# Kernel optimization log

Measured on AMD Instinct MI355X. Metric: run time of the kernel, lower is better.

## Reference

```python
import jax, jax.numpy as jnp
import numpy as np

L2 = (0.01, 0.01)
L1_RATIO = 0.5
EPS = 1e-16


def soft_thresholding(x, t):
    return jnp.sign(x) * jnp.maximum(jnp.abs(x) - t, 0.0)


def update_u(x, u, v, l1, l2, eps=EPS):
    # x: [B,M,N], u: [B,M,R], v: [B,N,R]
    a = jnp.einsum('bmn,bnr->bmr', x, v)      # x @ v            [B,M,R]
    b = jnp.einsum('bnr,bns->brs', v, v)      # v.mT @ v         [B,R,R]
    R = u.shape[-1]

    def step(u_new, r):
        # Gauss-Seidel update of column r using the freshest u_new (sequential dependency)
        br = jnp.take(b, r, axis=-1)                        # b[..., :, r]   [B,R]
        brr = jnp.take(br, r, axis=-1)                      # b[..., r, r]   [B]
        # term2 = u_new[..., indices] @ b[..., indices, r] computed as full matvec minus the r-th term
        term2 = jnp.einsum('bmk,bk->bm', u_new, br) - jnp.take(u_new, r, axis=-1) * brr[:, None]
        num = soft_thresholding(jnp.take(a, r, axis=-1) - term2, l1)   # [B,M]
        den = brr[:, None] + l2                                        # [B,1]
        ur = (num + eps) / (den + eps)
        return u_new.at[..., r].set(ur), None

    u_new, _ = jax.lax.scan(step, u, jnp.arange(R))
    return u_new


def setup_inputs() -> dict:
    key = jax.random.key(0)
    k1, k2, k3 = jax.random.split(key, 3)
    B, M, N, R = 8, 2048, 2048, 32
    x = jax.random.normal(k1, (B, M, N), dtype=jnp.float32)
    u = jax.random.normal(k2, (B, M, R), dtype=jnp.float32)
    v = jax.random.normal(k3, (B, N, R), dtype=jnp.float32)
    return {"x": x, "u": u, "v": v}


def reference(x, u, v):
    M, N = x.shape[-2], x.shape[-1]
    l1_u = L2[0] * L1_RATIO * N
    l2_u = L2[0] * (1.0 - L1_RATIO) * N
    l1_v = L2[1] * L1_RATIO * M
    l2_v = L2[1] * (1.0 - L1_RATIO) * M
    u = update_u(x, u, v, l1_u, l2_u)                              # factor 0
    v = update_u(jnp.swapaxes(x, -1, -2), v, u, l1_v, l2_v)        # factor 1 (update_v)
    return (u, v)
```

## Files before the change

### kernel.cpp

```cpp
#include <hip/hip_runtime.h>
#include <hip/hip_bf16.h>

#define NB 8
#define MD 2048
#define RD 32
#define KSPLIT 4
#define KSL (2048 / KSPLIT)
#define VT_STRIDE 520
#define XT_STRIDE 40

typedef float floatx4 __attribute__((ext_vector_type(4)));
typedef short shortx8 __attribute__((ext_vector_type(8)));

static __device__ __forceinline__ short f2b(float f) {
    __hip_bfloat16 h = __float2bfloat16(f);
    return (short)*reinterpret_cast<unsigned short*>(&h);
}

__global__ __launch_bounds__(256) void bmat_kernel(const float* __restrict__ w,
                                                   float* __restrict__ bmat) {
    int batch = blockIdx.x >> 5;
    int n0 = (blockIdx.x & 31) * 64;
    int t = threadIdx.x;
    __shared__ float ws[64][36];
    const float* wb = w + ((size_t)batch * 2048 + n0) * RD;
#pragma unroll
    for (int i = 0; i < 8; ++i) {
        int idx = t + i * 256;
        ws[idx >> 5][idx & 31] = wb[(idx >> 5) * RD + (idx & 31)];
    }
    __syncthreads();
    int ii = t >> 3;
    int jq = (t & 7) * 4;
    float acc[4] = {0.f, 0.f, 0.f, 0.f};
    for (int n = 0; n < 64; ++n) {
        float wi = ws[n][ii];
        float4 wj = *(const float4*)&ws[n][jq];
        acc[0] = fmaf(wi, wj.x, acc[0]);
        acc[1] = fmaf(wi, wj.y, acc[1]);
        acc[2] = fmaf(wi, wj.z, acc[2]);
        acc[3] = fmaf(wi, wj.w, acc[3]);
    }
    float* bp = bmat + ((size_t)batch * RD + ii) * RD + jq;
#pragma unroll
    for (int c = 0; c < 4; ++c) atomicAdd(bp + c, acc[c]);
}

__global__ __launch_bounds__(256, 4) void gemm1_kernel(const float* __restrict__ x,
                                                       const float* __restrict__ v,
                                                       float* __restrict__ a) {
    __shared__ short wT[32 * VT_STRIDE];
    int bz = blockIdx.x;
    int ks = bz & (KSPLIT - 1);
    int mblk = (bz >> 2) & 31;
    int batch = bz >> 7;
    int t = threadIdx.x;
    int lane = t & 63;
    int wave = t >> 6;

    const float* wb = v + ((size_t)batch * 2048 + ks * KSL) * RD;
#pragma unroll
    for (int i = 0; i < 16; ++i) {
        int idx = t + i * 256;
        int k = idx >> 3;
        int rq = (idx & 7) * 4;
        float4 f = *(const float4*)(wb + (size_t)k * RD + rq);
        wT[(rq + 0) * VT_STRIDE + k] = f2b(f.x);
        wT[(rq + 1) * VT_STRIDE + k] = f2b(f.y);
        wT[(rq + 2) * VT_STRIDE + k] = f2b(f.z);
        wT[(rq + 3) * VT_STRIDE + k] = f2b(f.w);
    }
    __syncthreads();

    int kq = (lane >> 4) * 8;
    const float* xrow =
        x + ((size_t)batch * MD + mblk * 64 + wave * 16 + (lane & 15)) * 2048 + ks * KSL + kq;
    int r0 = (lane & 15) * VT_STRIDE + kq;
    int r1 = ((lane & 15) + 16) * VT_STRIDE + kq;

    floatx4 acc0 = {0.f, 0.f, 0.f, 0.f}, acc1 = {0.f, 0.f, 0.f, 0.f};
    float4 fa = *(const float4*)(xrow);
    float4 fb = *(const float4*)(xrow + 4);
    for (int s = 0; s < KSL / 32; ++s) {
        float4 na = {0, 0, 0, 0}, nb = {0, 0, 0, 0};
        if (s + 1 < KSL / 32) {
            na = *(const float4*)(xrow + (s + 1) * 32);
            nb = *(const float4*)(xrow + (s + 1) * 32 + 4);
        }
        shortx8 af = {f2b(fa.x), f2b(fa.y), f2b(fa.z), f2b(fa.w),
                      f2b(fb.x), f2b(fb.y), f2b(fb.z), f2b(fb.w)};
        shortx8 b0 = *(const shortx8*)&wT[r0 + s * 32];
        shortx8 b1 = *(const shortx8*)&wT[r1 + s * 32];
        acc0 = __builtin_amdgcn_mfma_f32_16x16x32_bf16(af, b0, acc0, 0, 0, 0);
        acc1 = __builtin_amdgcn_mfma_f32_16x16x32_bf16(af, b1, acc1, 0, 0, 0);
        fa = na;
        fb = nb;
    }
    float* ab = a + ((size_t)batch * 2048 + mblk * 64 + wave * 16 + (lane >> 4) * 4) * RD + (lane & 15);
#pragma unroll
    for (int i = 0; i < 4; ++i) {
        atomicAdd(ab + i * RD, acc0[i]);
        atomicAdd(ab + i * RD + 16, acc1[i]);
    }
}

__global__ __launch_bounds__(256, 4) void gemm2_kernel(const float* __restrict__ x,
                                                       const float* __restrict__ u,
                                                       float* __restrict__ a) {
    __shared__ short uT[32 * VT_STRIDE];
    __shared__ short xT[4 * 16 * XT_STRIDE];
    int bz = blockIdx.x;
    int ks = bz & (KSPLIT - 1);
    int nblk = (bz >> 2) & 31;
    int batch = bz >> 7;
    int t = threadIdx.x;
    int lane = t & 63;
    int wave = t >> 6;

    const float* ub = u + ((size_t)batch * 2048 + ks * KSL) * RD;
#pragma unroll
    for (int i = 0; i < 16; ++i) {
        int idx = t + i * 256;
        int k = idx >> 3;
        int rq = (idx & 7) * 4;
        float4 f = *(const float4*)(ub + (size_t)k * RD + rq);
        uT[(rq + 0) * VT_STRIDE + k] = f2b(f.x);
        uT[(rq + 1) * VT_STRIDE + k] = f2b(f.y);
        uT[(rq + 2) * VT_STRIDE + k] = f2b(f.z);
        uT[(rq + 3) * VT_STRIDE + k] = f2b(f.w);
    }
    __syncthreads();

    short* xTw = &xT[wave * 16 * XT_STRIDE];
    int mloc = lane & 31;
    int ng = (lane >> 5) * 8;
    int n0w = nblk * 64 + wave * 16;
    const float* xp = x + ((size_t)batch * 2048 + ks * KSL + mloc) * 2048 + n0w + ng;

    int nl = lane & 15;
    int kq = (lane >> 4) * 8;
    int rA = nl * XT_STRIDE + kq;
    int rB0 = nl * VT_STRIDE + kq;
    int rB1 = (nl + 16) * VT_STRIDE + kq;

    floatx4 acc0 = {0.f, 0.f, 0.f, 0.f}, acc1 = {0.f, 0.f, 0.f, 0.f};
    float4 fa = *(const float4*)xp;
    float4 fb = *(const float4*)(xp + 4);
    for (int s = 0; s < KSL / 32; ++s) {
        xTw[(ng + 0) * XT_STRIDE + mloc] = f2b(fa.x);
        xTw[(ng + 1) * XT_STRIDE + mloc] = f2b(fa.y);
        xTw[(ng + 2) * XT_STRIDE + mloc] = f2b(fa.z);
        xTw[(ng + 3) * XT_STRIDE + mloc] = f2b(fa.w);
        xTw[(ng + 4) * XT_STRIDE + mloc] = f2b(fb.x);
        xTw[(ng + 5) * XT_STRIDE + mloc] = f2b(fb.y);
        xTw[(ng + 6) * XT_STRIDE + mloc] = f2b(fb.z);
        xTw[(ng + 7) * XT_STRIDE + mloc] = f2b(fb.w);
        float4 na = {0, 0, 0, 0}, nb = {0, 0, 0, 0};
        if (s + 1 < KSL / 32) {
            na = *(const float4*)(xp + (size_t)(s + 1) * 32 * 2048);
            nb = *(const float4*)(xp + (size_t)(s + 1) * 32 * 2048 + 4);
        }
        shortx8 af = *(const shortx8*)&xTw[rA];
        shortx8 b0 = *(const shortx8*)&uT[rB0 + s * 32];
        shortx8 b1 = *(const shortx8*)&uT[rB1 + s * 32];
        acc0 = __builtin_amdgcn_mfma_f32_16x16x32_bf16(af, b0, acc0, 0, 0, 0);
        acc1 = __builtin_amdgcn_mfma_f32_16x16x32_bf16(af, b1, acc1, 0, 0, 0);
        fa = na;
        fb = nb;
    }
    float* ab = a + ((size_t)batch * 2048 + n0w + (lane >> 4) * 4) * RD + (lane & 15);
#pragma unroll
    for (int i = 0; i < 4; ++i) {
        atomicAdd(ab + i * RD, acc0[i]);
        atomicAdd(ab + i * RD + 16, acc1[i]);
    }
}

__global__ __launch_bounds__(256) void gs_kernel(const float* __restrict__ uin,
                                                 const float* __restrict__ amat,
                                                 const float* __restrict__ bmat,
                                                 float* __restrict__ uout,
                                                 float l1, float l2) {
    int blk = blockIdx.x;
    int batch = blk >> 3;
    int m = (blk & 7) * 256 + threadIdx.x;
    __shared__ float bs[RD][RD];
    ((float4*)&bs[0][0])[threadIdx.x] =
        ((const float4*)(bmat + (size_t)batch * RD * RD))[threadIdx.x];
    __syncthreads();
    float uv[RD], av[RD];
    const float* up = uin + ((size_t)batch * 2048 + m) * RD;
    const float* ap = amat + ((size_t)batch * 2048 + m) * RD;
#pragma unroll
    for (int q = 0; q < 8; ++q) {
        *(float4*)&uv[q * 4] = *(const float4*)&up[q * 4];
        *(float4*)&av[q * 4] = *(const float4*)&ap[q * 4];
    }
#pragma unroll
    for (int r = 0; r < RD; ++r) {
        float brr = bs[r][r];
        float t2 = -uv[r] * brr;
#pragma unroll
        for (int k = 0; k < RD; ++k) t2 = fmaf(uv[k], bs[r][k], t2);
        float num = av[r] - t2;
        float mag = fmaxf(fabsf(num) - l1, 0.f);
        num = copysignf(mag, num);
        uv[r] = (num + 1e-16f) / (brr + l2 + 1e-16f);
    }
    float* op = uout + ((size_t)batch * 2048 + m) * RD;
#pragma unroll
    for (int q = 0; q < 8; ++q) *(float4*)&op[q * 4] = *(float4*)&uv[q * 4];
}

extern "C" void kernel_launch(void* const* d_in, const int* in_sizes, int n_in,
                              void* d_out, int out_size, void* d_ws, size_t ws_size,
                              hipStream_t stream) {
    const float* x = (const float*)d_in[0];
    const float* u = (const float*)d_in[1];
    const float* v = (const float*)d_in[2];
    float* out_u = (float*)d_out;
    float* out_v = out_u + (size_t)NB * MD * RD;
    float* a_ws = (float*)d_ws;
    float* b_ws = a_ws + (size_t)NB * 2048 * RD;
    const float l1u = 10.24f, l2u = 10.24f;
    const float l1v = 10.24f, l2v = 10.24f;
    size_t abytes = (size_t)NB * 2048 * RD * sizeof(float);
    size_t bbytes = (size_t)NB * RD * RD * sizeof(float);

    hipMemsetAsync(a_ws, 0, abytes + bbytes, stream);
    bmat_kernel<<<NB * 32, 256, 0, stream>>>(v, b_ws);
    gemm1_kernel<<<NB * 32 * KSPLIT, 256, 0, stream>>>(x, v, a_ws);
    gs_kernel<<<NB * 8, 256, 0, stream>>>(u, a_ws, b_ws, out_u, l1u, l2u);

    hipMemsetAsync(a_ws, 0, abytes + bbytes, stream);
    bmat_kernel<<<NB * 32, 256, 0, stream>>>(out_u, b_ws);
    gemm2_kernel<<<NB * 32 * KSPLIT, 256, 0, stream>>>(x, out_u, a_ws);
    gs_kernel<<<NB * 8, 256, 0, stream>>>(v, a_ws, b_ws, out_v, l1v, l2v);
}
```

Baseline: 255.2 us.

## Fuse Gram and GEMM kernels, replace atomics with split-K partial buffers

Merges the Gram-matrix kernel into the GEMM launch by giving the first blocks the bmat work, so the separate bmat kernel and memsets go away. Split-K partials for a and per-slice Gram partials are written with plain stores to separate buffers instead of atomics, and the Gauss-Seidel kernel sums them when it loads them. The GS inner dot product also gets four independent accumulators over float4 LDS reads. This costs more workspace and more reads in the GS kernel, and changes the floating-point summation order.

Measured after the change: 253.7 us (median of 2 runs). Within noise of the previous version (-0.6%).

```diff
diff --git a/kernel.cpp b/kernel.cpp
--- a/kernel.cpp
+++ b/kernel.cpp
@@ -8,6 +8,7 @@
 #define KSL (2048 / KSPLIT)
 #define VT_STRIDE 520
 #define XT_STRIDE 40
+#define ASL ((size_t)NB * 2048 * RD)
 
 typedef float floatx4 __attribute__((ext_vector_type(4)));
 typedef short shortx8 __attribute__((ext_vector_type(8)));
@@ -17,44 +18,50 @@
     return (short)*reinterpret_cast<unsigned short*>(&h);
 }
 
-__global__ __launch_bounds__(256) void bmat_kernel(const float* __restrict__ w,
-                                                   float* __restrict__ bmat) {
-    int batch = blockIdx.x >> 5;
-    int n0 = (blockIdx.x & 31) * 64;
-    int t = threadIdx.x;
-    __shared__ float ws[64][36];
-    const float* wb = w + ((size_t)batch * 2048 + n0) * RD;
+static __device__ __forceinline__ void bmat_part(const float* __restrict__ w,
+                                                 float* __restrict__ bp,
+                                                 int bz, int t, char* smem) {
+    int batch = bz >> 5;
+    int slice = bz & 31;
+    float* ws = (float*)smem;
+    const float* wb = w + ((size_t)batch * 2048 + slice * 64) * RD;
 #pragma unroll
     for (int i = 0; i < 8; ++i) {
         int idx = t + i * 256;
-        ws[idx >> 5][idx & 31] = wb[(idx >> 5) * RD + (idx & 31)];
+        ws[(idx >> 5) * 36 + (idx & 31)] = wb[(idx >> 5) * RD + (idx & 31)];
     }
     __syncthreads();
     int ii = t >> 3;
     int jq = (t & 7) * 4;
-    float acc[4] = {0.f, 0.f, 0.f, 0.f};
+    float a0 = 0.f, a1 = 0.f, a2 = 0.f, a3 = 0.f;
     for (int n = 0; n < 64; ++n) {
-        float wi = ws[n][ii];
-        float4 wj = *(const float4*)&ws[n][jq];
-        acc[0] = fmaf(wi, wj.x, acc[0]);
-        acc[1] = fmaf(wi, wj.y, acc[1]);
-        acc[2] = fmaf(wi, wj.z, acc[2]);
-        acc[3] = fmaf(wi, wj.w, acc[3]);
-    }
-    float* bp = bmat + ((size_t)batch * RD + ii) * RD + jq;
-#pragma unroll
-    for (int c = 0; c < 4; ++c) atomicAdd(bp + c, acc[c]);
-}
-
-__global__ __launch_bounds__(256, 4) void gemm1_kernel(const float* __restrict__ x,
-                                                       const float* __restrict__ v,
-                                                       float* __restrict__ a) {
-    __shared__ short wT[32 * VT_STRIDE];
+        float wi = ws[n * 36 + ii];
+        float4 wj = *(const float4*)&ws[n * 36 + jq];
+        a0 = fmaf(wi, wj.x, a0);
+        a1 = fmaf(wi, wj.y, a1);
+        a2 = fmaf(wi, wj.z, a2);
+        a3 = fmaf(wi, wj.w, a3);
+    }
+    float4 r = {a0, a1, a2, a3};
+    *(float4*)(bp + (((size_t)batch * 32 + slice) * RD + ii) * RD + jq) = r;
+}
+
+__global__ __launch_bounds__(256, 4) void fused1_kernel(const float* __restrict__ x,
+                                                        const float* __restrict__ v,
+                                                        float* __restrict__ ap,
+                                                        float* __restrict__ bp) {
+    __shared__ __align__(16) char smem[32 * VT_STRIDE * 2];
     int bz = blockIdx.x;
+    int t = threadIdx.x;
+    if (bz < NB * 32) {
+        bmat_part(v, bp, bz, t, smem);
+        return;
+    }
+    bz -= NB * 32;
+    short* wT = (short*)smem;
     int ks = bz & (KSPLIT - 1);
     int mblk = (bz >> 2) & 31;
     int batch = bz >> 7;
-    int t = threadIdx.x;
     int lane = t & 63;
     int wave = t >> 6;
 
@@ -96,24 +103,33 @@
         fa = na;
         fb = nb;
     }
-    float* ab = a + ((size_t)batch * 2048 + mblk * 64 + wave * 16 + (lane >> 4) * 4) * RD + (lane & 15);
+    float* ab = ap + ks * ASL +
+                ((size_t)batch * 2048 + mblk * 64 + wave * 16 + (lane >> 4) * 4) * RD +
+                (lane & 15);
 #pragma unroll
     for (int i = 0; i < 4; ++i) {
-        atomicAdd(ab + i * RD, acc0[i]);
-        atomicAdd(ab + i * RD + 16, acc1[i]);
-    }
-}
-
-__global__ __launch_bounds__(256, 4) void gemm2_kernel(const float* __restrict__ x,
-                                                       const float* __restrict__ u,
-                                                       float* __restrict__ a) {
-    __shared__ short uT[32 * VT_STRIDE];
-    __shared__ short xT[4 * 16 * XT_STRIDE];
+        ab[i * RD] = acc0[i];
+        ab[i * RD + 16] = acc1[i];
+    }
+}
+
+__global__ __launch_bounds__(256, 4) void fused2_kernel(const float* __restrict__ x,
+                                                        const float* __restrict__ u,
+                                                        float* __restrict__ ap,
+                                                        float* __restrict__ bp) {
+    __shared__ __align__(16) short smem[32 * VT_STRIDE + 4 * 16 * XT_STRIDE];
     int bz = blockIdx.x;
+    int t = threadIdx.x;
+    if (bz < NB * 32) {
+        bmat_part(u, bp, bz, t, (char*)smem);
+        return;
+    }
+    bz -= NB * 32;
+    short* uT = smem;
+    short* xT = smem + 32 * VT_STRIDE;
     int ks = bz & (KSPLIT - 1);
     int nblk = (bz >> 2) & 31;
     int batch = bz >> 7;
-    int t = threadIdx.x;
     int lane = t & 63;
     int wave = t >> 6;
 
@@ -168,40 +184,68 @@
         fa = na;
         fb = nb;
     }
-    float* ab = a + ((size_t)batch * 2048 + n0w + (lane >> 4) * 4) * RD + (lane & 15);
+    float* ab = ap + ks * ASL +
+                ((size_t)batch * 2048 + n0w + (lane >> 4) * 4) * RD + (lane & 15);
 #pragma unroll
     for (int i = 0; i < 4; ++i) {
-        atomicAdd(ab + i * RD, acc0[i]);
-        atomicAdd(ab + i * RD + 16, acc1[i]);
+        ab[i * RD] = acc0[i];
+        ab[i * RD + 16] = acc1[i];
     }
 }
 
 __global__ __launch_bounds__(256) void gs_kernel(const float* __restrict__ uin,
-                                                 const float* __restrict__ amat,
-                                                 const float* __restrict__ bmat,
+                                                 const float* __restrict__ ap,
+                                                 const float* __restrict__ bp,
                                                  float* __restrict__ uout,
                                                  float l1, float l2) {
     int blk = blockIdx.x;
     int batch = blk >> 3;
     int m = (blk & 7) * 256 + threadIdx.x;
     __shared__ float bs[RD][RD];
-    ((float4*)&bs[0][0])[threadIdx.x] =
-        ((const float4*)(bmat + (size_t)batch * RD * RD))[threadIdx.x];
+    {
+        const float4* bpp = (const float4*)(bp + (size_t)batch * 32 * RD * RD) + threadIdx.x;
+        float4 bacc = {0.f, 0.f, 0.f, 0.f};
+#pragma unroll
+        for (int s = 0; s < 32; ++s) {
+            float4 f = bpp[s * 256];
+            bacc.x += f.x;
+            bacc.y += f.y;
+            bacc.z += f.z;
+            bacc.w += f.w;
+        }
+        ((float4*)&bs[0][0])[threadIdx.x] = bacc;
+    }
     __syncthreads();
     float uv[RD], av[RD];
     const float* up = uin + ((size_t)batch * 2048 + m) * RD;
-    const float* ap = amat + ((size_t)batch * 2048 + m) * RD;
+    const float* app = ap + ((size_t)batch * 2048 + m) * RD;
 #pragma unroll
     for (int q = 0; q < 8; ++q) {
         *(float4*)&uv[q * 4] = *(const float4*)&up[q * 4];
-        *(float4*)&av[q * 4] = *(const float4*)&ap[q * 4];
+        float4 s0 = *(const float4*)(app + q * 4);
+        float4 s1 = *(const float4*)(app + ASL + q * 4);
+        float4 s2 = *(const float4*)(app + 2 * ASL + q * 4);
+        float4 s3 = *(const float4*)(app + 3 * ASL + q * 4);
+        float4 r;
+        r.x = (s0.x + s1.x) + (s2.x + s3.x);
+        r.y = (s0.y + s1.y) + (s2.y + s3.y);
+        r.z = (s0.z + s1.z) + (s2.z + s3.z);
+        r.w = (s0.w + s1.w) + (s2.w + s3.w);
+        *(float4*)&av[q * 4] = r;
     }
 #pragma unroll
     for (int r = 0; r < RD; ++r) {
         float brr = bs[r][r];
-        float t2 = -uv[r] * brr;
-#pragma unroll
-        for (int k = 0; k < RD; ++k) t2 = fmaf(uv[k], bs[r][k], t2);
+        float4 t2v = {0.f, 0.f, 0.f, 0.f};
+#pragma unroll
+        for (int q = 0; q < 8; ++q) {
+            float4 bq = *(const float4*)&bs[r][q * 4];
+            t2v.x = fmaf(uv[q * 4 + 0], bq.x, t2v.x);
+            t2v.y = fmaf(uv[q * 4 + 1], bq.y, t2v.y);
+            t2v.z = fmaf(uv[q * 4 + 2], bq.z, t2v.z);
+            t2v.w = fmaf(uv[q * 4 + 3], bq.w, t2v.w);
+        }
+        float t2 = ((t2v.x + t2v.y) + (t2v.z + t2v.w)) - uv[r] * brr;
         float num = av[r] - t2;
         float mag = fmaxf(fabsf(num) - l1, 0.f);
         num = copysignf(mag, num);
@@ -220,20 +264,15 @@
     const float* v = (const float*)d_in[2];
     float* out_u = (float*)d_out;
     float* out_v = out_u + (size_t)NB * MD * RD;
-    float* a_ws = (float*)d_ws;
-    float* b_ws = a_ws + (size_t)NB * 2048 * RD;
+    float* ap = (float*)d_ws;
+    float* bp = ap + KSPLIT * ASL;
     const float l1u = 10.24f, l2u = 10.24f;
     const float l1v = 10.24f, l2v = 10.24f;
-    size_t abytes = (size_t)NB * 2048 * RD * sizeof(float);
-    size_t bbytes = (size_t)NB * RD * RD * sizeof(float);
-
-    hipMemsetAsync(a_ws, 0, abytes + bbytes, stream);
-    bmat_kernel<<<NB * 32, 256, 0, stream>>>(v, b_ws);
-    gemm1_kernel<<<NB * 32 * KSPLIT, 256, 0, stream>>>(x, v, a_ws);
-    gs_kernel<<<NB * 8, 256, 0, stream>>>(u, a_ws, b_ws, out_u, l1u, l2u);
-
-    hipMemsetAsync(a_ws, 0, abytes + bbytes, stream);
-    bmat_kernel<<<NB * 32, 256, 0, stream>>>(out_u, b_ws);
-    gemm2_kernel<<<NB * 32 * KSPLIT, 256, 0, stream>>>(x, out_u, a_ws);
-    gs_kernel<<<NB * 8, 256, 0, stream>>>(v, a_ws, b_ws, out_v, l1v, l2v);
-}
+    const int GRID = NB * 32 + NB * 32 * KSPLIT;
+
+    fused1_kernel<<<GRID, 256, 0, stream>>>(x, v, ap, bp);
+    gs_kernel<<<NB * 8, 256, 0, stream>>>(u, ap, bp, out_u, l1u, l2u);
+
+    fused2_kernel<<<GRID, 256, 0, stream>>>(x, out_u, ap, bp);
+    gs_kernel<<<NB * 8, 256, 0, stream>>>(v, ap, bp, out_v, l1v, l2v);
+}
```
